# Performance work log

Hardware: AMD Instinct MI355X
Metric: run time of the kernel (lower is better)

The kernel has to match this reference:

```python
import jax, jax.numpy as jnp
import numpy as np

D_MODEL = 1024
D_INNER = 2048
D_STATE = 16
D_CONV = 4
DT_RANK = 64
BATCH = 2
SEQLEN = 1024


def setup_inputs() -> dict:
    key = jax.random.key(0)
    ks = jax.random.split(key, 12)
    s = 0.02
    # dt bias initialized as inverse-softplus of dt ~ LogUniform(1e-3, 1e-1), as in the torch code
    dt = jnp.exp(jax.random.uniform(ks[7], (D_INNER,)) * (np.log(0.1) - np.log(0.001)) + np.log(0.001))
    dt = jnp.clip(dt, 1e-4, None)
    inv_dt = jnp.log(jnp.expm1(dt))
    A_log = jnp.log(jnp.broadcast_to(jnp.arange(1, D_STATE + 1, dtype=jnp.float32), (D_INNER, D_STATE)))
    return {
        "hidden_states": jax.random.normal(ks[0], (BATCH, SEQLEN, D_MODEL), jnp.float32),
        "x_text": jax.random.normal(ks[1], (BATCH, D_MODEL), jnp.float32),
        "in_proj_w": jax.random.normal(ks[2], (2 * D_INNER, D_MODEL), jnp.float32) * s,
        "conv_w": jax.random.normal(ks[3], (D_INNER, 1, D_CONV), jnp.float32) * s,
        "conv_b": jax.random.normal(ks[4], (D_INNER,), jnp.float32) * s,
        "x_proj_w": jax.random.normal(ks[5], (DT_RANK + 2 * D_STATE, D_INNER), jnp.float32) * s,
        "dt_proj_w": jax.random.normal(ks[6], (D_INNER, DT_RANK), jnp.float32) * (DT_RANK ** -0.5),
        "dt_proj_b": inv_dt.astype(jnp.float32),
        "A_log": A_log.astype(jnp.float32),
        "D": jnp.ones((D_INNER,), jnp.float32),
        "out_proj_w": jax.random.normal(ks[8], (D_MODEL, D_INNER), jnp.float32) * s,
        "gate_w": jax.random.normal(ks[9], (DT_RANK + 2 * D_STATE, D_MODEL), jnp.float32) * s,
        "gate_b": jnp.zeros((DT_RANK + 2 * D_STATE,), jnp.float32),
    }


def _causal_depthwise_conv(x, w, b):
    # x: (b, d, l), w: (d, 1, k) depthwise, left-pad k-1 for causality
    y = jax.lax.conv_general_dilated(
        x, w, window_strides=(1,), padding=[(D_CONV - 1, 0)],
        dimension_numbers=("NCH", "OIH", "NCH"), feature_group_count=D_INNER)
    return y + b[None, :, None]


def _mamba_forward(hidden_states, x_text, in_proj_w, conv_w, conv_b, x_proj_w,
                   dt_proj_w, dt_proj_b, A_log, D, out_proj_w, gate_w, gate_b):
    b = hidden_states.shape[0]
    # input projection -> x, z each (b, l, d_inner)
    xz = jnp.einsum("bld,ed->ble", hidden_states, in_proj_w)
    x, z = jnp.split(xz, 2, axis=-1)
    # causal depthwise conv + SiLU
    xc = _causal_depthwise_conv(jnp.transpose(x, (0, 2, 1)), conv_w, conv_b)
    xc = jnp.transpose(jax.nn.silu(xc), (0, 2, 1))  # (b, l, d_inner)
    # x_proj -> dt/B/C, modulated by text gate
    x_dbl = jnp.einsum("bld,ed->ble", xc, x_proj_w)  # (b, l, dt_rank+2n)
    gate = jax.nn.sigmoid(x_text @ gate_w.T + gate_b)  # (b, dt_rank+2n)
    x_dbl = x_dbl * gate[:, None, :]
    dt, Bm, Cm = jnp.split(x_dbl, [DT_RANK, DT_RANK + D_STATE], axis=-1)
    delta = jax.nn.softplus(jnp.einsum("blr,dr->bld", dt, dt_proj_w) + dt_proj_b)  # (b, l, d)
    A = -jnp.exp(A_log)  # (d, n)
    dA = jnp.exp(jnp.einsum("bld,dn->bldn", delta, A))          # (b, l, d, n)
    dBx = jnp.einsum("bld,bln->bldn", delta * xc, Bm)            # (b, l, d, n)

    def step(h, inp):
        dA_t, dBx_t, C_t = inp
        h = h * dA_t + dBx_t                       # (b, d, n)
        y_t = jnp.einsum("bdn,bn->bd", h, C_t)
        return h, y_t

    h0 = jnp.zeros((b, D_INNER, D_STATE), delta.dtype)
    _, ys = jax.lax.scan(step, h0, (jnp.transpose(dA, (1, 0, 2, 3)),
                                    jnp.transpose(dBx, (1, 0, 2, 3)),
                                    jnp.transpose(Cm, (1, 0, 2))))
    y = jnp.transpose(ys, (1, 0, 2)) + D * xc      # (b, l, d_inner)
    y = y * jax.nn.silu(z)
    return jnp.einsum("bld,md->blm", y, out_proj_w)


def reference(hidden_states, x_text, in_proj_w, conv_w, conv_b, x_proj_w,
              dt_proj_w, dt_proj_b, A_log, D, out_proj_w, gate_w, gate_b):
    return _mamba_forward(hidden_states, x_text, in_proj_w, conv_w, conv_b, x_proj_w,
                          dt_proj_w, dt_proj_b, A_log, D, out_proj_w, gate_w, gate_b)
```

## Files before the change

kernel.cpp:

```cpp
#include <hip/hip_runtime.h>

#define BATCH   2
#define SEQLEN  1024
#define DMODEL  1024
#define DINNER  2048
#define DSTATE  16
#define DCONV   4
#define DTRANK  64
#define GDIM    96
#define MROWS   (BATCH*SEQLEN)

#define NCHUNK  64
#define LCHUNK  16
#define SPLITX  16
#define SPLITO  2

typedef __attribute__((ext_vector_type(8))) short bf16x8_t;
typedef __attribute__((ext_vector_type(4))) float f32x4_t;
typedef __attribute__((ext_vector_type(4))) unsigned short u16x4_t;
typedef unsigned short ushort_t;

__device__ __forceinline__ unsigned short f2bf(float x) {
    union { float f; unsigned int u; } v; v.f = x;
    unsigned int r = v.u + 0x7FFFu + ((v.u >> 16) & 1u);
    return (unsigned short)(r >> 16);
}
__device__ __forceinline__ float bf2f(unsigned short h) {
    union { unsigned int u; float f; } v; v.u = ((unsigned int)h) << 16;
    return v.f;
}

__device__ __forceinline__ void gload_lds16(const ushort_t* g, short* l) {
    __builtin_amdgcn_global_load_lds(
        (const __attribute__((address_space(1))) unsigned int*)g,
        (__attribute__((address_space(3))) unsigned int*)l, 16, 0, 0);
}

#define N1 (MROWS*DMODEL)
#define N2 (2*DINNER*DMODEL)
#define N3 (GDIM*DINNER)
#define N4 (DINNER*DTRANK)
#define N5 (DMODEL*DINNER)
#define NTOT (N1+N2+N3+N4+N5)
__global__ __launch_bounds__(256)
void cvt5_kernel(const float* __restrict__ s1, const float* __restrict__ s2,
                 const float* __restrict__ s3, const float* __restrict__ s4,
                 const float* __restrict__ s5,
                 ushort_t* o1, ushort_t* o2, ushort_t* o3, ushort_t* o4, ushort_t* o5) {
    int idx = (blockIdx.x * 256 + threadIdx.x) * 4;
    if (idx >= NTOT) return;
    const float* src; ushort_t* dst;
    if (idx < N1)              { src = s1; dst = o1; }
    else if ((idx -= N1) < N2) { src = s2; dst = o2; }
    else if ((idx -= N2) < N3) { src = s3; dst = o3; }
    else if ((idx -= N3) < N4) { src = s4; dst = o4; }
    else                       { idx -= N4; src = s5; dst = o5; }
    f32x4_t v = *(const f32x4_t*)(src + idx);
    u16x4_t o;
    #pragma unroll
    for (int j = 0; j < 4; j++) o[j] = f2bf(v[j]);
    *(u16x4_t*)(dst + idx) = o;
}

template<int EPI>
__global__ __launch_bounds__(256)
void gemm_bf(const ushort_t* __restrict__ A, const ushort_t* __restrict__ W,
             void* __restrict__ out0, void* __restrict__ out1,
             const float* __restrict__ bias, int M, int N, int K) {
    __shared__ __align__(16) short As[2][128 * 32];
    __shared__ __align__(16) short Bs[2][128 * 32];

    const int tid  = threadIdx.x;
    const int m0   = blockIdx.x * 128;
    const int n0   = blockIdx.y * 128;
    const int klen = K / gridDim.z;
    const int kbeg = blockIdx.z * klen;

    const int w    = tid >> 6;
    const int lane = tid & 63;
    const int quad = lane >> 4;
    const int l15  = lane & 15;
    const int wm   = (w >> 1) * 64;
    const int wn   = (w & 1) * 64;

    const int rl  = lane >> 2;
    const int kc  = (((lane & 3) ^ ((lane >> 3) & 3)) << 3);
    const int arow0 = m0 + (w * 2 + 0) * 16 + rl;
    const int arow1 = m0 + (w * 2 + 1) * 16 + rl;
    int brow0 = n0 + (w * 2 + 0) * 16 + rl; if (brow0 > N - 1) brow0 = N - 1;
    int brow1 = n0 + (w * 2 + 1) * 16 + rl; if (brow1 > N - 1) brow1 = N - 1;

    const int sw = ((quad ^ ((l15 >> 1) & 3)) << 3);

    f32x4_t acc[4][4];
    #pragma unroll
    for (int i = 0; i < 4; i++)
        #pragma unroll
        for (int j = 0; j < 4; j++)
            acc[i][j] = (f32x4_t){0.f, 0.f, 0.f, 0.f};

    {
        const int kk = kbeg + kc;
        gload_lds16(A + (size_t)arow0 * K + kk, &As[0][(w * 2 + 0) * 512]);
        gload_lds16(A + (size_t)arow1 * K + kk, &As[0][(w * 2 + 1) * 512]);
        gload_lds16(W + (size_t)brow0 * K + kk, &Bs[0][(w * 2 + 0) * 512]);
        gload_lds16(W + (size_t)brow1 * K + kk, &Bs[0][(w * 2 + 1) * 512]);
    }

    int cur = 0;
    for (int k0 = 0; k0 < klen; k0 += 32) {
        if (k0 + 32 < klen) {
            const int kk = kbeg + k0 + 32 + kc;
            gload_lds16(A + (size_t)arow0 * K + kk, &As[cur ^ 1][(w * 2 + 0) * 512]);
            gload_lds16(A + (size_t)arow1 * K + kk, &As[cur ^ 1][(w * 2 + 1) * 512]);
            gload_lds16(W + (size_t)brow0 * K + kk, &Bs[cur ^ 1][(w * 2 + 0) * 512]);
            gload_lds16(W + (size_t)brow1 * K + kk, &Bs[cur ^ 1][(w * 2 + 1) * 512]);
            asm volatile("s_waitcnt vmcnt(4)" ::: "memory");
        } else {
            asm volatile("s_waitcnt vmcnt(0)" ::: "memory");
        }
        __builtin_amdgcn_sched_barrier(0);
        asm volatile("s_barrier" ::: "memory");
        __builtin_amdgcn_sched_barrier(0);

        bf16x8_t af[4], bfv[4];
        #pragma unroll
        for (int mi = 0; mi < 4; mi++)
            af[mi] = *(const bf16x8_t*)(&As[cur][(wm + mi * 16 + l15) * 32 + sw]);
        #pragma unroll
        for (int ni = 0; ni < 4; ni++)
            bfv[ni] = *(const bf16x8_t*)(&Bs[cur][(wn + ni * 16 + l15) * 32 + sw]);
        #pragma unroll
        for (int mi = 0; mi < 4; mi++)
            #pragma unroll
            for (int ni = 0; ni < 4; ni++)
                acc[mi][ni] = __builtin_amdgcn_mfma_f32_16x16x32_bf16(af[mi], bfv[ni], acc[mi][ni], 0, 0, 0);

        __builtin_amdgcn_sched_barrier(0);
        asm volatile("s_barrier" ::: "memory");
        __builtin_amdgcn_sched_barrier(0);
        cur ^= 1;
    }

    const size_t zoff = (size_t)blockIdx.z * M * N;
    #pragma unroll
    for (int mi = 0; mi < 4; mi++) {
        #pragma unroll
        for (int ni = 0; ni < 4; ni++) {
            #pragma unroll
            for (int r = 0; r < 4; r++) {
                int gm = m0 + wm + mi * 16 + quad * 4 + r;
                int gn = n0 + wn + ni * 16 + l15;
                if (gn < N) {
                    float v = acc[mi][ni][r];
                    if (EPI == 0) {
                        ((float*)out0)[zoff + (size_t)gm * N + gn] = v;
                    } else if (EPI == 1) {
                        float t = v + bias[gn];
                        float sp = (t > 20.f) ? t : log1pf(__expf(t));
                        ((ushort_t*)out0)[(size_t)gm * N + gn] = f2bf(sp);
                    } else {
                        if (gn < DINNER)
                            ((ushort_t*)out0)[(size_t)gm * DINNER + gn] = f2bf(v);
                        else
                            ((float*)out1)[(size_t)gm * DINNER + (gn - DINNER)] = v;
                    }
                }
            }
        }
    }
}

#define CONVBLK ((MROWS*DINNER)/256)
__global__ __launch_bounds__(256)
void convgate_kernel(const ushort_t* __restrict__ x,
                     const float* __restrict__ cw,
                     const float* __restrict__ cb,
                     ushort_t* __restrict__ xc,
                     const float* __restrict__ xt,
                     const float* __restrict__ gw,
                     const float* __restrict__ gb,
                     float* __restrict__ gate) {
    if (blockIdx.x < CONVBLK) {
        int idx = blockIdx.x * 256 + threadIdx.x;
        int d  = idx & (DINNER - 1);
        int bl = idx >> 11;
        int l  = bl & (SEQLEN - 1);
        float acc = cb[d];
        #pragma unroll
        for (int j = 0; j < DCONV; j++) {
            int lj = l - (DCONV - 1) + j;
            if (lj >= 0)
                acc += cw[d * DCONV + j] * bf2f(x[(size_t)(bl - (DCONV - 1) + j) * DINNER + d]);
        }
        float v = acc / (1.f + __expf(-acc));
        xc[idx] = f2bf(v);
    } else {
        int g = blockIdx.x - CONVBLK;
        int b = g / GDIM, j = g % GDIM;
        int tid = threadIdx.x;
        float s = 0.f;
        for (int k = tid; k < DMODEL; k += 256)
            s += xt[b * DMODEL + k] * gw[j * DMODEL + k];
        #pragma unroll
        for (int o = 32; o > 0; o >>= 1) s += __shfl_down(s, o);
        __shared__ float red[4];
        if ((tid & 63) == 0) red[tid >> 6] = s;
        __syncthreads();
        if (tid == 0) {
            float t = red[0] + red[1] + red[2] + red[3] + gb[j];
            gate[b * GDIM + j] = 1.f / (1.f + __expf(-t));
        }
    }
}

__global__ void gatemul_kernel(const float* __restrict__ xp,
                               const float* __restrict__ gate,
                               ushort_t* __restrict__ dt,
                               float* __restrict__ Bm,
                               float* __restrict__ Cm) {
    int idx = blockIdx.x * 256 + threadIdx.x;
    if (idx >= MROWS * GDIM) return;
    int j  = idx % GDIM;
    int bl = idx / GDIM;
    int b  = bl >> 10;
    float v = 0.f;
    #pragma unroll
    for (int z = 0; z < SPLITX; z++)
        v += xp[(size_t)z * MROWS * GDIM + idx];
    v *= gate[b * GDIM + j];
    if (j < DTRANK)               dt[bl * DTRANK + j] = f2bf(v);
    else if (j < DTRANK + DSTATE) Bm[bl * DSTATE + (j - DTRANK)] = v;
    else                          Cm[bl * DSTATE + (j - DTRANK - DSTATE)] = v;
}

__global__ __launch_bounds__(256)
void scan1_kernel(const ushort_t* __restrict__ delta,
                  const ushort_t* __restrict__ xc,
                  const float* __restrict__ Bm,
                  const float* __restrict__ A_log,
                  float* __restrict__ hfin,
                  float* __restrict__ dsum) {
    __shared__ float sBm[LCHUNK][DSTATE];
    int tid = threadIdx.x;
    int d = blockIdx.x * 256 + tid;
    int b = blockIdx.y;
    int c = blockIdx.z;
    int l0 = c * LCHUNK;
    for (int t = tid; t < LCHUNK * DSTATE; t += 256)
        sBm[t >> 4][t & 15] = Bm[((size_t)(b * SEQLEN + l0 + (t >> 4))) * DSTATE + (t & 15)];
    __syncthreads();

    float Ac[DSTATE];
    #pragma unroll
    for (int n = 0; n < DSTATE; n++)
        Ac[n] = -__expf(A_log[d * DSTATE + n]);
    float h[DSTATE];
    #pragma unroll
    for (int n = 0; n < DSTATE; n++) h[n] = 0.f;
    float ds = 0.f;

    for (int s = 0; s < LCHUNK; s++) {
        size_t ix = (size_t)(b * SEQLEN + l0 + s) * DINNER + d;
        float dv = bf2f(delta[ix]);
        float xv = bf2f(xc[ix]);
        float dx = dv * xv;
        ds += dv;
        #pragma unroll
        for (int n = 0; n < DSTATE; n++) {
            float e = __expf(dv * Ac[n]);
            h[n] = h[n] * e + dx * sBm[s][n];
        }
    }
    size_t base = ((size_t)(b * DINNER + d) * NCHUNK + c) * DSTATE;
    #pragma unroll
    for (int n = 0; n < DSTATE; n++) hfin[base + n] = h[n];
    dsum[((size_t)b * NCHUNK + c) * DINNER + d] = ds;
}

__global__ __launch_bounds__(256)
void scan2_kernel(float* __restrict__ hfin,
                  const float* __restrict__ dsum,
                  const float* __restrict__ A_log) {
    __shared__ float sh[NCHUNK * DSTATE];
    __shared__ float sp[NCHUNK * DSTATE];
    __shared__ float sAc[DSTATE];
    __shared__ float sds[NCHUNK];
    const int tid = threadIdx.x;
    const int bd  = blockIdx.x;
    const int b   = bd >> 11;
    const int d   = bd & (DINNER - 1);
    if (tid < DSTATE) sAc[tid] = -__expf(A_log[d * DSTATE + tid]);
    if (tid < NCHUNK) sds[tid] = dsum[((size_t)b * NCHUNK + tid) * DINNER + d];
    const size_t base = (size_t)bd * (NCHUNK * DSTATE);
    float hl[4];
    #pragma unroll
    for (int r = 0; r < 4; r++) hl[r] = hfin[base + tid + r * 256];
    __syncthreads();
    #pragma unroll
    for (int r = 0; r < 4; r++) {
        int i = tid + r * 256;
        sh[i] = hl[r];
        sp[i] = __expf(sAc[i & 15] * sds[i >> 4]);
    }
    __syncthreads();
    #pragma unroll
    for (int s = 1; s < NCHUNK; s <<= 1) {
        float nh[4], np[4];
        #pragma unroll
        for (int r = 0; r < 4; r++) {
            int i = tid + r * 256;
            int c = i >> 4;
            if (c >= s) {
                int j = i - (s << 4);
                nh[r] = sh[i] + sp[i] * sh[j];
                np[r] = sp[i] * sp[j];
            } else { nh[r] = sh[i]; np[r] = sp[i]; }
        }
        __syncthreads();
        #pragma unroll
        for (int r = 0; r < 4; r++) { int i = tid + r * 256; sh[i] = nh[r]; sp[i] = np[r]; }
        __syncthreads();
    }
    #pragma unroll
    for (int r = 0; r < 4; r++) {
        int i = tid + r * 256;
        hfin[base + i] = (i >> 4) ? sh[i - 16] : 0.f;
    }
}

__global__ __launch_bounds__(256)
void scan3_kernel(const ushort_t* __restrict__ delta,
                  ushort_t* __restrict__ xc,
                  const float* __restrict__ z,
                  const float* __restrict__ Bm,
                  const float* __restrict__ Cm,
                  const float* __restrict__ A_log,
                  const float* __restrict__ Dp,
                  const float* __restrict__ h0) {
    __shared__ float sBm[LCHUNK][DSTATE];
    __shared__ float sCm[LCHUNK][DSTATE];
    int tid = threadIdx.x;
    int d = blockIdx.x * 256 + tid;
    int b = blockIdx.y;
    int c = blockIdx.z;
    int l0 = c * LCHUNK;
    for (int t = tid; t < LCHUNK * DSTATE; t += 256) {
        size_t src = ((size_t)(b * SEQLEN + l0 + (t >> 4))) * DSTATE + (t & 15);
        sBm[t >> 4][t & 15] = Bm[src];
        sCm[t >> 4][t & 15] = Cm[src];
    }
    __syncthreads();

    float Ac[DSTATE];
    #pragma unroll
    for (int n = 0; n < DSTATE; n++)
        Ac[n] = -__expf(A_log[d * DSTATE + n]);

    float h[DSTATE];
    size_t hb0 = ((size_t)(b * DINNER + d) * NCHUNK + c) * DSTATE;
    #pragma unroll
    for (int n = 0; n < DSTATE; n++) h[n] = h0[hb0 + n];

    float Dv = Dp[d];

    for (int s = 0; s < LCHUNK; s++) {
        size_t ix = (size_t)(b * SEQLEN + l0 + s) * DINNER + d;
        float dv = bf2f(delta[ix]);
        float xv = bf2f(xc[ix]);
        float dx = dv * xv;
        float y = 0.f;
        #pragma unroll
        for (int n = 0; n < DSTATE; n++) {
            float e = __expf(dv * Ac[n]);
            h[n] = h[n] * e + dx * sBm[s][n];
            y += h[n] * sCm[s][n];
        }
        float zv = z[ix];
        float o = (y + Dv * xv) * (zv / (1.f + __expf(-zv)));
        xc[ix] = f2bf(o);
    }
}

__global__ void reduce2_kernel(const float* __restrict__ p, float* __restrict__ out, int n) {
    int i = blockIdx.x * 256 + threadIdx.x;
    if (i < n)
        out[i] = p[i] + p[(size_t)n + i];
}

extern "C" void kernel_launch(void* const* d_in, const int* in_sizes, int n_in,
                              void* d_out, int out_size, void* d_ws, size_t ws_size,
                              hipStream_t stream) {
    const float* hidden   = (const float*)d_in[0];
    const float* x_text   = (const float*)d_in[1];
    const float* in_proj  = (const float*)d_in[2];
    const float* conv_w   = (const float*)d_in[3];
    const float* conv_b   = (const float*)d_in[4];
    const float* x_proj   = (const float*)d_in[5];
    const float* dt_proj  = (const float*)d_in[6];
    const float* dt_bias  = (const float*)d_in[7];
    const float* A_log    = (const float*)d_in[8];
    const float* Dparam   = (const float*)d_in[9];
    const float* out_proj = (const float*)d_in[10];
    const float* gate_w   = (const float*)d_in[11];
    const float* gate_b   = (const float*)d_in[12];

    char* ws = (char*)d_ws;
    size_t off = 0;
    auto alloc = [&](size_t bytes) -> char* {
        char* p = ws + off;
        off += (bytes + 255) & ~(size_t)255;
        return p;
    };
    ushort_t* hb    = (ushort_t*)alloc((size_t)N1 * 2);
    ushort_t* w_in  = (ushort_t*)alloc((size_t)N2 * 2);
    ushort_t* w_x   = (ushort_t*)alloc((size_t)N3 * 2);
    ushort_t* w_dt  = (ushort_t*)alloc((size_t)N4 * 2);
    ushort_t* w_o   = (ushort_t*)alloc((size_t)N5 * 2);
    float*    X     = (float*)alloc((size_t)MROWS * DINNER * 4);
    float*    zbuf  = (float*)alloc((size_t)MROWS * DINNER * 4);
    float*    hfin  = (float*)alloc((size_t)BATCH * DINNER * NCHUNK * DSTATE * 4);
    float*    dsum  = (float*)alloc((size_t)BATCH * NCHUNK * DINNER * 4);
    float*    gate  = (float*)alloc((size_t)BATCH * GDIM * 4);
    float*    Bm    = (float*)alloc((size_t)MROWS * DSTATE * 4);
    float*    Cm    = (float*)alloc((size_t)MROWS * DSTATE * 4);
    ushort_t* dt    = (ushort_t*)alloc((size_t)MROWS * DTRANK * 2);

    ushort_t* xb    = (ushort_t*)X;
    ushort_t* xc    = w_in;
    ushort_t* delta = (ushort_t*)X;
    float*    xpart = hfin;
    float*    outp  = X;

    cvt5_kernel<<<(NTOT / 4 + 255) / 256, 256, 0, stream>>>(
        hidden, in_proj, x_proj, dt_proj, out_proj, hb, w_in, w_x, w_dt, w_o);

    gemm_bf<3><<<dim3(MROWS / 128, (2 * DINNER) / 128, 1), 256, 0, stream>>>(
        hb, w_in, xb, zbuf, nullptr, MROWS, 2 * DINNER, DMODEL);

    convgate_kernel<<<CONVBLK + BATCH * GDIM, 256, 0, stream>>>(
        xb, conv_w, conv_b, xc, x_text, gate_w, gate_b, gate);

    gemm_bf<0><<<dim3(MROWS / 128, 1, SPLITX), 256, 0, stream>>>(
        xc, w_x, xpart, nullptr, nullptr, MROWS, GDIM, DINNER);

    gatemul_kernel<<<(MROWS * GDIM + 255) / 256, 256, 0, stream>>>(
        xpart, gate, dt, Bm, Cm);

    gemm_bf<1><<<dim3(MROWS / 128, DINNER / 128, 1), 256, 0, stream>>>(
        dt, w_dt, delta, nullptr, dt_bias, MROWS, DINNER, DTRANK);

    scan1_kernel<<<dim3(DINNER / 256, BATCH, NCHUNK), 256, 0, stream>>>(
        delta, xc, Bm, A_log, hfin, dsum);

    scan2_kernel<<<BATCH * DINNER, 256, 0, stream>>>(hfin, dsum, A_log);

    scan3_kernel<<<dim3(DINNER / 256, BATCH, NCHUNK), 256, 0, stream>>>(
        delta, xc, zbuf, Bm, Cm, A_log, Dparam, hfin);

    gemm_bf<0><<<dim3(MROWS / 128, DMODEL / 128, SPLITO), 256, 0, stream>>>(
        xc, w_o, outp, nullptr, nullptr, MROWS, DMODEL, DINNER);

    reduce2_kernel<<<(MROWS * DMODEL + 255) / 256, 256, 0, stream>>>(
        outp, (float*)d_out, MROWS * DMODEL);
}
```

Before: 288.5 us.

## Fuse x_proj, gate, dt_proj and three scan phases into one cooperative kernel

Refactors the GEMM body into a device function so it can run inside a persistent cooperative kernel. That kernel runs the x_proj split-K GEMM, the gate multiply, the dt_proj GEMM and the three chunked-scan phases, separated by grid-wide syncs. This removes several kernel launches and inter-kernel gaps, at the cost of five grid barriers and a fixed 1024-block grid that must be co-resident. The in_proj epilogue now writes x in fp32 instead of bf16, and the conv kernel reads fp32. This adds memory traffic but removes one rounding step. The old multi-kernel path is kept as a fallback if the cooperative launch fails.

Result: slower. 840.4 us (+191.3%).

```diff
diff --git a/kernel.cpp b/kernel.cpp
--- a/kernel.cpp
+++ b/kernel.cpp
@@ -1,4 +1,7 @@
 #include <hip/hip_runtime.h>
+#include <hip/hip_cooperative_groups.h>
+
+namespace cg = cooperative_groups;
 
 #define BATCH   2
 #define SEQLEN  1024
@@ -63,18 +66,14 @@
 }
 
 template<int EPI>
-__global__ __launch_bounds__(256)
-void gemm_bf(const ushort_t* __restrict__ A, const ushort_t* __restrict__ W,
-             void* __restrict__ out0, void* __restrict__ out1,
-             const float* __restrict__ bias, int M, int N, int K) {
-    __shared__ __align__(16) short As[2][128 * 32];
-    __shared__ __align__(16) short Bs[2][128 * 32];
-
+__device__ __forceinline__ void gemm_dev(short* AsB, short* BsB,
+             const ushort_t* A, const ushort_t* W,
+             void* out0, void* out1, const float* bias,
+             int M, int N, int K, int bm, int bn, int bz, int klen) {
     const int tid  = threadIdx.x;
-    const int m0   = blockIdx.x * 128;
-    const int n0   = blockIdx.y * 128;
-    const int klen = K / gridDim.z;
-    const int kbeg = blockIdx.z * klen;
+    const int m0   = bm * 128;
+    const int n0   = bn * 128;
+    const int kbeg = bz * klen;
 
     const int w    = tid >> 6;
     const int lane = tid & 63;
@@ -101,20 +100,22 @@
 
     {
         const int kk = kbeg + kc;
-        gload_lds16(A + (size_t)arow0 * K + kk, &As[0][(w * 2 + 0) * 512]);
-        gload_lds16(A + (size_t)arow1 * K + kk, &As[0][(w * 2 + 1) * 512]);
-        gload_lds16(W + (size_t)brow0 * K + kk, &Bs[0][(w * 2 + 0) * 512]);
-        gload_lds16(W + (size_t)brow1 * K + kk, &Bs[0][(w * 2 + 1) * 512]);
+        gload_lds16(A + (size_t)arow0 * K + kk, AsB + (w * 2 + 0) * 512);
+        gload_lds16(A + (size_t)arow1 * K + kk, AsB + (w * 2 + 1) * 512);
+        gload_lds16(W + (size_t)brow0 * K + kk, BsB + (w * 2 + 0) * 512);
+        gload_lds16(W + (size_t)brow1 * K + kk, BsB + (w * 2 + 1) * 512);
     }
 
     int cur = 0;
     for (int k0 = 0; k0 < klen; k0 += 32) {
         if (k0 + 32 < klen) {
             const int kk = kbeg + k0 + 32 + kc;
-            gload_lds16(A + (size_t)arow0 * K + kk, &As[cur ^ 1][(w * 2 + 0) * 512]);
-            gload_lds16(A + (size_t)arow1 * K + kk, &As[cur ^ 1][(w * 2 + 1) * 512]);
-            gload_lds16(W + (size_t)brow0 * K + kk, &Bs[cur ^ 1][(w * 2 + 0) * 512]);
-            gload_lds16(W + (size_t)brow1 * K + kk, &Bs[cur ^ 1][(w * 2 + 1) * 512]);
+            short* An = AsB + (cur ^ 1) * 4096;
+            short* Bn = BsB + (cur ^ 1) * 4096;
+            gload_lds16(A + (size_t)arow0 * K + kk, An + (w * 2 + 0) * 512);
+            gload_lds16(A + (size_t)arow1 * K + kk, An + (w * 2 + 1) * 512);
+            gload_lds16(W + (size_t)brow0 * K + kk, Bn + (w * 2 + 0) * 512);
+            gload_lds16(W + (size_t)brow1 * K + kk, Bn + (w * 2 + 1) * 512);
             asm volatile("s_waitcnt vmcnt(4)" ::: "memory");
         } else {
             asm volatile("s_waitcnt vmcnt(0)" ::: "memory");
@@ -123,13 +124,15 @@
         asm volatile("s_barrier" ::: "memory");
         __builtin_amdgcn_sched_barrier(0);
 
+        const short* Ac_ = AsB + cur * 4096;
+        const short* Bc_ = BsB + cur * 4096;
         bf16x8_t af[4], bfv[4];
         #pragma unroll
         for (int mi = 0; mi < 4; mi++)
-            af[mi] = *(const bf16x8_t*)(&As[cur][(wm + mi * 16 + l15) * 32 + sw]);
+            af[mi] = *(const bf16x8_t*)(Ac_ + (wm + mi * 16 + l15) * 32 + sw);
         #pragma unroll
         for (int ni = 0; ni < 4; ni++)
-            bfv[ni] = *(const bf16x8_t*)(&Bs[cur][(wn + ni * 16 + l15) * 32 + sw]);
+            bfv[ni] = *(const bf16x8_t*)(Bc_ + (wn + ni * 16 + l15) * 32 + sw);
         #pragma unroll
         for (int mi = 0; mi < 4; mi++)
             #pragma unroll
@@ -142,7 +145,7 @@
         cur ^= 1;
     }
 
-    const size_t zoff = (size_t)blockIdx.z * M * N;
+    const size_t zoff = (size_t)bz * M * N;
     #pragma unroll
     for (int mi = 0; mi < 4; mi++) {
         #pragma unroll
@@ -161,7 +164,7 @@
                         ((ushort_t*)out0)[(size_t)gm * N + gn] = f2bf(sp);
                     } else {
                         if (gn < DINNER)
-                            ((ushort_t*)out0)[(size_t)gm * DINNER + gn] = f2bf(v);
+                            ((float*)out0)[(size_t)gm * DINNER + gn] = v;
                         else
                             ((float*)out1)[(size_t)gm * DINNER + (gn - DINNER)] = v;
                     }
@@ -171,9 +174,19 @@
     }
 }
 
+template<int EPI>
+__global__ __launch_bounds__(256)
+void gemm_bf(const ushort_t* __restrict__ A, const ushort_t* __restrict__ W,
+             void* __restrict__ out0, void* __restrict__ out1,
+             const float* __restrict__ bias, int M, int N, int K) {
+    __shared__ __align__(16) short smem[16384];
+    gemm_dev<EPI>(smem, smem + 8192, A, W, out0, out1, bias, M, N, K,
+                  blockIdx.x, blockIdx.y, blockIdx.z, K / gridDim.z);
+}
+
 #define CONVBLK ((MROWS*DINNER)/256)
 __global__ __launch_bounds__(256)
-void convgate_kernel(const ushort_t* __restrict__ x,
+void convgate_kernel(const float* __restrict__ x,
                      const float* __restrict__ cw,
                      const float* __restrict__ cb,
                      ushort_t* __restrict__ xc,
@@ -191,7 +204,7 @@
         for (int j = 0; j < DCONV; j++) {
             int lj = l - (DCONV - 1) + j;
             if (lj >= 0)
-                acc += cw[d * DCONV + j] * bf2f(x[(size_t)(bl - (DCONV - 1) + j) * DINNER + d]);
+                acc += cw[d * DCONV + j] * x[(size_t)(bl - (DCONV - 1) + j) * DINNER + d];
         }
         float v = acc / (1.f + __expf(-acc));
         xc[idx] = f2bf(v);
@@ -214,20 +227,189 @@
     }
 }
 
-__global__ void gatemul_kernel(const float* __restrict__ xp,
-                               const float* __restrict__ gate,
-                               ushort_t* __restrict__ dt,
-                               float* __restrict__ Bm,
+__global__ __launch_bounds__(256, 4)
+void mega_kernel(const ushort_t* xc_in, ushort_t* xc,
+                 const ushort_t* w_x, float* xpart,
+                 const float* gate, ushort_t* dtb, float* Bm, float* Cm,
+                 const ushort_t* w_dt, ushort_t* delta, const float* dt_bias,
+                 const float* A_log, const float* Dp, const float* zbuf,
+                 float* hfin, float* dsum) {
+    __shared__ __align__(16) short smem[16384];
+    cg::grid_group grid = cg::this_grid();
+    const int tid = threadIdx.x;
+    const int bx  = blockIdx.x;
+    short* As = smem;
+    short* Bs = smem + 8192;
+
+    if (bx < 256)
+        gemm_dev<0>(As, Bs, xc_in, w_x, xpart, nullptr, nullptr,
+                    MROWS, GDIM, DINNER, bx & 15, 0, bx >> 4, DINNER / SPLITX);
+    grid.sync();
+
+    {
+        int idx = bx * 256 + tid;
+        if (idx < MROWS * GDIM) {
+            int j  = idx % GDIM;
+            int bl = idx / GDIM;
+            int b  = bl >> 10;
+            float v = 0.f;
+            #pragma unroll
+            for (int z = 0; z < SPLITX; z++)
+                v += xpart[(size_t)z * MROWS * GDIM + idx];
+            v *= gate[b * GDIM + j];
+            if (j < DTRANK)               dtb[bl * DTRANK + j] = f2bf(v);
+            else if (j < DTRANK + DSTATE) Bm[bl * DSTATE + (j - DTRANK)] = v;
+            else                          Cm[bl * DSTATE + (j - DTRANK - DSTATE)] = v;
+        }
+    }
+    grid.sync();
+
+    if (bx < 256)
+        gemm_dev<1>(As, Bs, dtb, w_dt, delta, nullptr, dt_bias,
+                    MROWS, DINNER, DTRANK, bx & 15, bx >> 4, 0, DTRANK);
+    grid.sync();
+
+    const int dblk = bx & 7;
+    const int b_   = (bx >> 3) & 1;
+    const int c_   = bx >> 4;
+    const int d_   = dblk * 256 + tid;
+    const int l0   = c_ * LCHUNK;
+
+    {
+        float* sBm = (float*)smem;
+        for (int t = tid; t < LCHUNK * DSTATE; t += 256)
+            sBm[t] = Bm[((size_t)(b_ * SEQLEN + l0 + (t >> 4))) * DSTATE + (t & 15)];
+        __syncthreads();
+
+        float Ac[DSTATE];
+        #pragma unroll
+        for (int n = 0; n < DSTATE; n++)
+            Ac[n] = -__expf(A_log[d_ * DSTATE + n]);
+        float h[DSTATE];
+        #pragma unroll
+        for (int n = 0; n < DSTATE; n++) h[n] = 0.f;
+        float ds = 0.f;
+
+        for (int s = 0; s < LCHUNK; s++) {
+            size_t ix = (size_t)(b_ * SEQLEN + l0 + s) * DINNER + d_;
+            float dv = bf2f(delta[ix]);
+            float xv = bf2f(xc_in[ix]);
+            float dx = dv * xv;
+            ds += dv;
+            #pragma unroll
+            for (int n = 0; n < DSTATE; n++) {
+                float e = __expf(dv * Ac[n]);
+                h[n] = h[n] * e + dx * sBm[(s << 4) + n];
+            }
+        }
+        size_t base = ((size_t)(b_ * DINNER + d_) * NCHUNK + c_) * DSTATE;
+        #pragma unroll
+        for (int n = 0; n < DSTATE; n++) hfin[base + n] = h[n];
+        dsum[((size_t)b_ * NCHUNK + c_) * DINNER + d_] = ds;
+    }
+    grid.sync();
+
+    {
+        float* sh  = (float*)smem;
+        float* sp  = sh + 1024;
+        float* sAc = sp + 1024;
+        float* sds = sAc + 16;
+        for (int it = 0; it < 4; ++it) {
+            int bd = it * 1024 + bx;
+            int bb = bd >> 11;
+            int dd = bd & (DINNER - 1);
+            if (tid < DSTATE) sAc[tid] = -__expf(A_log[dd * DSTATE + tid]);
+            if (tid < NCHUNK) sds[tid] = dsum[((size_t)bb * NCHUNK + tid) * DINNER + dd];
+            const size_t base = (size_t)bd * (NCHUNK * DSTATE);
+            float hl[4];
+            #pragma unroll
+            for (int r = 0; r < 4; r++) hl[r] = hfin[base + tid + r * 256];
+            __syncthreads();
+            #pragma unroll
+            for (int r = 0; r < 4; r++) {
+                int i = tid + r * 256;
+                sh[i] = hl[r];
+                sp[i] = __expf(sAc[i & 15] * sds[i >> 4]);
+            }
+            __syncthreads();
+            #pragma unroll
+            for (int s = 1; s < NCHUNK; s <<= 1) {
+                float nh[4], np[4];
+                #pragma unroll
+                for (int r = 0; r < 4; r++) {
+                    int i = tid + r * 256;
+                    int c = i >> 4;
+                    if (c >= s) {
+                        int j = i - (s << 4);
+                        nh[r] = sh[i] + sp[i] * sh[j];
+                        np[r] = sp[i] * sp[j];
+                    } else { nh[r] = sh[i]; np[r] = sp[i]; }
+                }
+                __syncthreads();
+                #pragma unroll
+                for (int r = 0; r < 4; r++) { int i = tid + r * 256; sh[i] = nh[r]; sp[i] = np[r]; }
+                __syncthreads();
+            }
+            #pragma unroll
+            for (int r = 0; r < 4; r++) {
+                int i = tid + r * 256;
+                hfin[base + i] = (i >> 4) ? sh[i - 16] : 0.f;
+            }
+            __syncthreads();
+        }
+    }
+    grid.sync();
+
+    {
+        float* sBm = (float*)smem;
+        float* sCm = sBm + 256;
+        for (int t = tid; t < LCHUNK * DSTATE; t += 256) {
+            size_t src = ((size_t)(b_ * SEQLEN + l0 + (t >> 4))) * DSTATE + (t & 15);
+            sBm[t] = Bm[src];
+            sCm[t] = Cm[src];
+        }
+        __syncthreads();
+
+        float Ac[DSTATE];
+        #pragma unroll
+        for (int n = 0; n < DSTATE; n++)
+            Ac[n] = -__expf(A_log[d_ * DSTATE + n]);
+
+        float h[DSTATE];
+        size_t hb0 = ((size_t)(b_ * DINNER + d_) * NCHUNK + c_) * DSTATE;
+        #pragma unroll
+        for (int n = 0; n < DSTATE; n++) h[n] = hfin[hb0 + n];
+
+        float Dv = Dp[d_];
+
+        for (int s = 0; s < LCHUNK; s++) {
+            size_t ix = (size_t)(b_ * SEQLEN + l0 + s) * DINNER + d_;
+            float dv = bf2f(delta[ix]);
+            float xv = bf2f(xc_in[ix]);
+            float dx = dv * xv;
+            float y = 0.f;
+            #pragma unroll
+            for (int n = 0; n < DSTATE; n++) {
+                float e = __expf(dv * Ac[n]);
+                h[n] = h[n] * e + dx * sBm[(s << 4) + n];
+                y += h[n] * sCm[(s << 4) + n];
+            }
+            float zv = zbuf[ix];
+            float o = (y + Dv * xv) * (zv / (1.f + __expf(-zv)));
+            xc[ix] = f2bf(o);
+        }
+    }
+}
+
+__global__ void gatemul_kernel(const float* __restrict__ xp, const float* __restrict__ gate,
+                               ushort_t* __restrict__ dt, float* __restrict__ Bm,
                                float* __restrict__ Cm) {
     int idx = blockIdx.x * 256 + threadIdx.x;
     if (idx >= MROWS * GDIM) return;
-    int j  = idx % GDIM;
-    int bl = idx / GDIM;
-    int b  = bl >> 10;
+    int j = idx % GDIM, bl = idx / GDIM, b = bl >> 10;
     float v = 0.f;
     #pragma unroll
-    for (int z = 0; z < SPLITX; z++)
-        v += xp[(size_t)z * MROWS * GDIM + idx];
+    for (int z = 0; z < SPLITX; z++) v += xp[(size_t)z * MROWS * GDIM + idx];
     v *= gate[b * GDIM + j];
     if (j < DTRANK)               dt[bl * DTRANK + j] = f2bf(v);
     else if (j < DTRANK + DSTATE) Bm[bl * DSTATE + (j - DTRANK)] = v;
@@ -235,35 +417,26 @@
 }
 
 __global__ __launch_bounds__(256)
-void scan1_kernel(const ushort_t* __restrict__ delta,
-                  const ushort_t* __restrict__ xc,
-                  const float* __restrict__ Bm,
-                  const float* __restrict__ A_log,
-                  float* __restrict__ hfin,
-                  float* __restrict__ dsum) {
+void scan1_kernel(const ushort_t* __restrict__ delta, const ushort_t* __restrict__ xc,
+                  const float* __restrict__ Bm, const float* __restrict__ A_log,
+                  float* __restrict__ hfin, float* __restrict__ dsum) {
     __shared__ float sBm[LCHUNK][DSTATE];
     int tid = threadIdx.x;
-    int d = blockIdx.x * 256 + tid;
-    int b = blockIdx.y;
-    int c = blockIdx.z;
+    int d = blockIdx.x * 256 + tid, b = blockIdx.y, c = blockIdx.z;
     int l0 = c * LCHUNK;
     for (int t = tid; t < LCHUNK * DSTATE; t += 256)
         sBm[t >> 4][t & 15] = Bm[((size_t)(b * SEQLEN + l0 + (t >> 4))) * DSTATE + (t & 15)];
     __syncthreads();
-
     float Ac[DSTATE];
     #pragma unroll
-    for (int n = 0; n < DSTATE; n++)
-        Ac[n] = -__expf(A_log[d * DSTATE + n]);
+    for (int n = 0; n < DSTATE; n++) Ac[n] = -__expf(A_log[d * DSTATE + n]);
     float h[DSTATE];
     #pragma unroll
     for (int n = 0; n < DSTATE; n++) h[n] = 0.f;
     float ds = 0.f;
-
     for (int s = 0; s < LCHUNK; s++) {
         size_t ix = (size_t)(b * SEQLEN + l0 + s) * DINNER + d;
-        float dv = bf2f(delta[ix]);
-        float xv = bf2f(xc[ix]);
+        float dv = bf2f(delta[ix]), xv = bf2f(xc[ix]);
         float dx = dv * xv;
         ds += dv;
         #pragma unroll
@@ -279,17 +452,11 @@
 }
 
 __global__ __launch_bounds__(256)
-void scan2_kernel(float* __restrict__ hfin,
-                  const float* __restrict__ dsum,
+void scan2_kernel(float* __restrict__ hfin, const float* __restrict__ dsum,
                   const float* __restrict__ A_log) {
-    __shared__ float sh[NCHUNK * DSTATE];
-    __shared__ float sp[NCHUNK * DSTATE];
-    __shared__ float sAc[DSTATE];
-    __shared__ float sds[NCHUNK];
-    const int tid = threadIdx.x;
-    const int bd  = blockIdx.x;
-    const int b   = bd >> 11;
-    const int d   = bd & (DINNER - 1);
+    __shared__ float sh[NCHUNK * DSTATE], sp[NCHUNK * DSTATE], sAc[DSTATE], sds[NCHUNK];
+    const int tid = threadIdx.x, bd = blockIdx.x;
+    const int b = bd >> 11, d = bd & (DINNER - 1);
     if (tid < DSTATE) sAc[tid] = -__expf(A_log[d * DSTATE + tid]);
     if (tid < NCHUNK) sds[tid] = dsum[((size_t)b * NCHUNK + tid) * DINNER + d];
     const size_t base = (size_t)bd * (NCHUNK * DSTATE);
@@ -309,8 +476,7 @@
         float nh[4], np[4];
         #pragma unroll
         for (int r = 0; r < 4; r++) {
-            int i = tid + r * 256;
-            int c = i >> 4;
+            int i = tid + r * 256, c = i >> 4;
             if (c >= s) {
                 int j = i - (s << 4);
                 nh[r] = sh[i] + sp[i] * sh[j];
@@ -330,20 +496,13 @@
 }
 
 __global__ __launch_bounds__(256)
-void scan3_kernel(const ushort_t* __restrict__ delta,
-                  ushort_t* __restrict__ xc,
-                  const float* __restrict__ z,
-                  const float* __restrict__ Bm,
-                  const float* __restrict__ Cm,
-                  const float* __restrict__ A_log,
-                  const float* __restrict__ Dp,
-                  const float* __restrict__ h0) {
-    __shared__ float sBm[LCHUNK][DSTATE];
-    __shared__ float sCm[LCHUNK][DSTATE];
+void scan3_kernel(const ushort_t* __restrict__ delta, ushort_t* __restrict__ xc,
+                  const float* __restrict__ z, const float* __restrict__ Bm,
+                  const float* __restrict__ Cm, const float* __restrict__ A_log,
+                  const float* __restrict__ Dp, const float* __restrict__ h0) {
+    __shared__ float sBm[LCHUNK][DSTATE], sCm[LCHUNK][DSTATE];
     int tid = threadIdx.x;
-    int d = blockIdx.x * 256 + tid;
-    int b = blockIdx.y;
-    int c = blockIdx.z;
+    int d = blockIdx.x * 256 + tid, b = blockIdx.y, c = blockIdx.z;
     int l0 = c * LCHUNK;
     for (int t = tid; t < LCHUNK * DSTATE; t += 256) {
         size_t src = ((size_t)(b * SEQLEN + l0 + (t >> 4))) * DSTATE + (t & 15);
@@ -351,23 +510,17 @@
         sCm[t >> 4][t & 15] = Cm[src];
     }
     __syncthreads();
-
     float Ac[DSTATE];
     #pragma unroll
-    for (int n = 0; n < DSTATE; n++)
-        Ac[n] = -__expf(A_log[d * DSTATE + n]);
-
+    for (int n = 0; n < DSTATE; n++) Ac[n] = -__expf(A_log[d * DSTATE + n]);
     float h[DSTATE];
     size_t hb0 = ((size_t)(b * DINNER + d) * NCHUNK + c) * DSTATE;
     #pragma unroll
     for (int n = 0; n < DSTATE; n++) h[n] = h0[hb0 + n];
-
     float Dv = Dp[d];
-
     for (int s = 0; s < LCHUNK; s++) {
         size_t ix = (size_t)(b * SEQLEN + l0 + s) * DINNER + d;
-        float dv = bf2f(delta[ix]);
-        float xv = bf2f(xc[ix]);
+        float dv = bf2f(delta[ix]), xv = bf2f(xc[ix]);
         float dx = dv * xv;
         float y = 0.f;
         #pragma unroll
@@ -426,7 +579,6 @@
     float*    Cm    = (float*)alloc((size_t)MROWS * DSTATE * 4);
     ushort_t* dt    = (ushort_t*)alloc((size_t)MROWS * DTRANK * 2);
 
-    ushort_t* xb    = (ushort_t*)X;
     ushort_t* xc    = w_in;
     ushort_t* delta = (ushort_t*)X;
     float*    xpart = hfin;
@@ -436,27 +588,36 @@
         hidden, in_proj, x_proj, dt_proj, out_proj, hb, w_in, w_x, w_dt, w_o);
 
     gemm_bf<3><<<dim3(MROWS / 128, (2 * DINNER) / 128, 1), 256, 0, stream>>>(
-        hb, w_in, xb, zbuf, nullptr, MROWS, 2 * DINNER, DMODEL);
+        hb, w_in, X, zbuf, nullptr, MROWS, 2 * DINNER, DMODEL);
 
     convgate_kernel<<<CONVBLK + BATCH * GDIM, 256, 0, stream>>>(
-        xb, conv_w, conv_b, xc, x_text, gate_w, gate_b, gate);
-
-    gemm_bf<0><<<dim3(MROWS / 128, 1, SPLITX), 256, 0, stream>>>(
-        xc, w_x, xpart, nullptr, nullptr, MROWS, GDIM, DINNER);
-
-    gatemul_kernel<<<(MROWS * GDIM + 255) / 256, 256, 0, stream>>>(
-        xpart, gate, dt, Bm, Cm);
-
-    gemm_bf<1><<<dim3(MROWS / 128, DINNER / 128, 1), 256, 0, stream>>>(
-        dt, w_dt, delta, nullptr, dt_bias, MROWS, DINNER, DTRANK);
-
-    scan1_kernel<<<dim3(DINNER / 256, BATCH, NCHUNK), 256, 0, stream>>>(
-        delta, xc, Bm, A_log, hfin, dsum);
-
-    scan2_kernel<<<BATCH * DINNER, 256, 0, stream>>>(hfin, dsum, A_log);
-
-    scan3_kernel<<<dim3(DINNER / 256, BATCH, NCHUNK), 256, 0, stream>>>(
-        delta, xc, zbuf, Bm, Cm, A_log, Dparam, hfin);
+        X, conv_w, conv_b, xc, x_text, gate_w, gate_b, gate);
+
+    {
+        const ushort_t* xc_c = xc;
+        void* args[] = {
+            (void*)&xc_c, (void*)&xc, (void*)&w_x, (void*)&xpart,
+            (void*)&gate, (void*)&dt, (void*)&Bm, (void*)&Cm,
+            (void*)&w_dt, (void*)&delta, (void*)&dt_bias,
+            (void*)&A_log, (void*)&Dparam, (void*)&zbuf,
+            (void*)&hfin, (void*)&dsum
+        };
+        hipError_t err = hipLaunchCooperativeKernel(
+            reinterpret_cast<void*>(mega_kernel), dim3(1024), dim3(256), args, 0, stream);
+        if (err != hipSuccess) {
+            gemm_bf<0><<<dim3(MROWS / 128, 1, SPLITX), 256, 0, stream>>>(
+                xc, w_x, xpart, nullptr, nullptr, MROWS, GDIM, DINNER);
+            gatemul_kernel<<<(MROWS * GDIM + 255) / 256, 256, 0, stream>>>(
+                xpart, gate, dt, Bm, Cm);
+            gemm_bf<1><<<dim3(MROWS / 128, DINNER / 128, 1), 256, 0, stream>>>(
+                dt, w_dt, delta, nullptr, dt_bias, MROWS, DINNER, DTRANK);
+            scan1_kernel<<<dim3(DINNER / 256, BATCH, NCHUNK), 256, 0, stream>>>(
+                delta, xc, Bm, A_log, hfin, dsum);
+            scan2_kernel<<<BATCH * DINNER, 256, 0, stream>>>(hfin, dsum, A_log);
+            scan3_kernel<<<dim3(DINNER / 256, BATCH, NCHUNK), 256, 0, stream>>>(
+                delta, xc, zbuf, Bm, Cm, A_log, Dparam, hfin);
+        }
+    }
 
     gemm_bf<0><<<dim3(MROWS / 128, DMODEL / 128, SPLITO), 256, 0, stream>>>(
         xc, w_o, outp, nullptr, nullptr, MROWS, DMODEL, DINNER);
```
